# Kernel optimization log

Hardware: AMD Instinct MI355X
Metric: run time of the kernel (lower is better)

## Reference

```python
import jax, jax.numpy as jnp
import numpy as np

DIMS = 1024
HEAD = 16
HD = DIMS // HEAD          # head_dim = 64
LAYER = 2
STRIDE = max(1, 6 - LAYER)  # skip-path k/v stride = 4
EPS = 1.1920929e-07         # torch.finfo(float32).eps (RMSNorm eps=None default)


def rmsnorm(x, w):
    # torch nn.RMSNorm over last dim with affine weight
    ms = jnp.mean(jnp.square(x), axis=-1, keepdims=True)
    return x * jax.lax.rsqrt(ms + EPS) * w


def rope_freqs(seq_len):
    # rotary._compute_freqs with mask=None, x=None (mel-style scale)
    end = 2595.0 * np.log10(1.0 + 4000.0 / 200.0)
    scale = jnp.power(10.0, jnp.linspace(0.0, end, HD // 2, dtype=jnp.float32) / 2595.0) - 1.0
    base = 200.0 * scale / 1000.0                      # [HD//2]
    t = jnp.arange(seq_len, dtype=jnp.float32)          # [c]
    return t[:, None] * base[None, :]                   # [c, HD//2]


def rope(x, freqs):
    # x: [b,h,c,d]; interleaved pairs rotated by angle freqs[c, d//2]
    xr = x.reshape(*x.shape[:-1], HD // 2, 2)
    a, b = xr[..., 0], xr[..., 1]
    cos, sin = jnp.cos(freqs), jnp.sin(freqs)           # broadcast over [b,h]
    out = jnp.stack([a * cos - b * sin, a * sin + b * cos], axis=-1)
    return out.reshape(x.shape)


def setup_inputs() -> dict:
    key = jax.random.key(0)
    ks = jax.random.split(key, 4)
    d = DIMS
    init = lambda k, shape: jax.random.normal(k, shape, jnp.float32) * 0.02
    return {
        "x": jax.random.normal(ks[0], (4, 2048, d), jnp.float32),
        "rmsq_w": jnp.ones((d,), jnp.float32),
        "q_w": init(ks[1], (d, d)),
        "q_b": jnp.zeros((d,), jnp.float32),
        "rmskv_w": jnp.ones((d,), jnp.float32),
        "kv_w": init(ks[2], (d, 2 * d)),
        "kv_b": jnp.zeros((2 * d,), jnp.float32),
        "ln_w": jnp.ones((HD,), jnp.float32),
        "out_w": init(ks[3], (d, d)),
        "out_b": jnp.zeros((d,), jnp.float32),
    }


def reference(x, rmsq_w, q_w, q_b, rmskv_w, kv_w, kv_b, ln_w, out_w, out_b):
    b, c, d = x.shape
    # q = RMSNorm -> Linear -> [b,h,c,hd]
    q = (rmsnorm(x, rmsq_w) @ q_w + q_b).reshape(b, c, HEAD, HD).transpose(0, 2, 1, 3)
    # kv = RMSNorm -> Linear(d,2d) -> split last dim as (kv=2, h, hd)
    kv = (rmsnorm(x, rmskv_w) @ kv_w + kv_b).reshape(b, c, 2, HEAD, HD)
    k = kv[:, :, 0].transpose(0, 2, 1, 3)  # [b,h,c,hd]
    v = kv[:, :, 1].transpose(0, 2, 1, 3)
    # rotary embedding (full hd rotated since freqs cover hd//2 pairs)
    freqs = rope_freqs(c)
    q = rope(q, freqs)
    k = rope(k, freqs)
    # skip branch: strided subsampling of k/v (stride = max(1, 6-layer) = 4)
    k = k[:, :, ::STRIDE, :]
    v = v[:, :, ::STRIDE, :]
    # per-head RMSNorm on q/k, then SDPA (is_causal=False since mask=None)
    qn = rmsnorm(q, ln_w)
    kn = rmsnorm(k, ln_w)
    scores = jnp.einsum('bhqd,bhkd->bhqk', qn, kn) / jnp.sqrt(jnp.float32(HD))
    a = jnp.einsum('bhqk,bhkd->bhqd', jax.nn.softmax(scores, axis=-1), v)
    # out projection: [b,h,c,hd] -> [b,c,d] -> Linear
    out = a.transpose(0, 2, 1, 3).reshape(b, c, d) @ out_w + out_b
    return out
```

## Files before the change

### kernel.cpp

```cpp
#include <hip/hip_runtime.h>

#define EPSF 1.1920929e-07f
#define QSCALE 0.18033688011112042f

typedef _Float16 hf;
typedef __attribute__((ext_vector_type(4))) _Float16 h4;
typedef __attribute__((ext_vector_type(8))) _Float16 h8;
typedef __attribute__((ext_vector_type(4))) float fx4;

#define DEVI __device__ __forceinline__

DEVI void async16(const void* g, void* l) {
  __builtin_amdgcn_global_load_lds((const __attribute__((address_space(1))) unsigned int*)g,
                                   (__attribute__((address_space(3))) unsigned int*)l, 16, 0, 0);
}

DEVI fx4 mfma16(h4 a, h4 b, fx4 c) {
  return __builtin_amdgcn_mfma_f32_16x16x16f16(a, b, c, 0, 0, 0);
}
DEVI fx4 mfma32(h8 a, h8 b, fx4 c) {
  return __builtin_amdgcn_mfma_f32_16x16x32_f16(a, b, c, 0, 0, 0);
}

DEVI h8 ld16(const hf* base, int row, int g16) {
  int off = (row * 128 + (g16 << 4)) ^ ((row & 7) << 4);
  return *(const h8*)((const char*)base + off);
}
DEVI h4 ld8(const hf* base, int row, int g8) {
  int off = (row * 128 + (g8 << 3)) ^ ((row & 7) << 4);
  return *(const h4*)((const char*)base + off);
}

__global__ __launch_bounds__(256) void k_wcast(const float* __restrict__ W, hf* __restrict__ Wt,
                                               int K, int N) {
  __shared__ float ls[64][65];
  int kt = blockIdx.x, nt = blockIdx.y, t = threadIdx.x;
  int c4 = (t & 15) * 4, r0 = t >> 4;
#pragma unroll
  for (int i = 0; i < 4; ++i) {
    int row = i * 16 + r0;
    fx4 v = *(const fx4*)(W + (size_t)(kt * 64 + row) * N + nt * 64 + c4);
    ls[row][c4 + 0] = v[0]; ls[row][c4 + 1] = v[1];
    ls[row][c4 + 2] = v[2]; ls[row][c4 + 3] = v[3];
  }
  __syncthreads();
  int cc = t >> 4, kk4 = (t & 15) * 4;
#pragma unroll
  for (int i = 0; i < 4; ++i) {
    int nn = i * 16 + cc;
    h4 p = {(hf)ls[kk4 + 0][nn], (hf)ls[kk4 + 1][nn], (hf)ls[kk4 + 2][nn], (hf)ls[kk4 + 3][nn]};
    *(h4*)(Wt + (size_t)(nt * 64 + nn) * K + kt * 64 + kk4) = p;
  }
}

__global__ __launch_bounds__(256) void k_table(float* __restrict__ tab) {
  int idx = blockIdx.x * 256 + threadIdx.x;
  int tt = idx >> 5, j = idx & 31;
  double e = pow(21.0, (double)j / 31.0) - 1.0;
  float bf = (float)(0.2 * e);
  float fr = (float)tt * bf;
  double d = (double)fr;
  float2 cs = make_float2((float)cos(d), (float)sin(d));
  ((float2*)tab)[idx] = cs;
}

__global__ __launch_bounds__(256) void k_dualnorm(const float* __restrict__ x,
                                                  const float* __restrict__ wq,
                                                  const float* __restrict__ wkv,
                                                  hf* __restrict__ xqn, hf* __restrict__ xkvc) {
  int row = blockIdx.x, t = threadIdx.x;
  const fx4* xr = (const fx4*)(x + (size_t)row * 1024);
  fx4 v = xr[t];
  float ss = v[0] * v[0] + v[1] * v[1] + v[2] * v[2] + v[3] * v[3];
#pragma unroll
  for (int m = 1; m <= 32; m <<= 1) ss += __shfl_xor(ss, m);
  __shared__ float red[4];
  if ((t & 63) == 0) red[t >> 6] = ss;
  __syncthreads();
  float r = rsqrtf((red[0] + red[1] + red[2] + red[3]) * (1.0f / 1024.0f) + EPSF);
  fx4 a = ((const fx4*)wq)[t];
  h4 oq = {(hf)(v[0] * r * a[0]), (hf)(v[1] * r * a[1]), (hf)(v[2] * r * a[2]), (hf)(v[3] * r * a[3])};
  *(h4*)(xqn + (size_t)row * 1024 + t * 4) = oq;
  int c = row & 2047;
  if ((c & 3) == 0) {
    fx4 bk = ((const fx4*)wkv)[t];
    int crow = (row >> 11) * 512 + (c >> 2);
    h4 ok = {(hf)(v[0] * r * bk[0]), (hf)(v[1] * r * bk[1]), (hf)(v[2] * r * bk[2]), (hf)(v[3] * r * bk[3])};
    *(h4*)(xkvc + (size_t)crow * 1024 + t * 4) = ok;
  }
}

template <int EPI>
__global__ __launch_bounds__(256) void k_gemm(const hf* __restrict__ A, const hf* __restrict__ Bt,
                                              const float* __restrict__ bias, void* __restrict__ outp,
                                              int M, int N, int K, int MB, hf* __restrict__ vt) {
  __shared__ alignas(16) hf lsA[2][128 * 64];
  __shared__ alignas(16) hf lsB[2][128 * 64];
  int t = threadIdx.x, l = t & 63, w = t >> 6, grp = l >> 4, ln = l & 15;
  int bm = blockIdx.x % MB, bn = blockIdx.x / MB;
  int m0 = bm * 128, n0 = bn * 128;
  int wr = w >> 1, wc = w & 1;
  fx4 acc[4][4] = {};
  int nkt = K >> 6;

  auto stage = [&](int kt, int b) {
    int k0 = kt << 6;
#pragma unroll
    for (int p = 0; p < 4; ++p) {
      int ci = p * 256 + t;
      int row = ci >> 3, g = (ci & 7) ^ (row & 7);
      async16(A + (size_t)(m0 + row) * K + k0 + g * 8, (char*)lsA[b] + p * 4096 + w * 1024);
    }
#pragma unroll
    for (int p = 0; p < 4; ++p) {
      int ci = p * 256 + t;
      int row = ci >> 3, g = (ci & 7) ^ (row & 7);
      async16(Bt + (size_t)(n0 + row) * K + k0 + g * 8, (char*)lsB[b] + p * 4096 + w * 1024);
    }
  };

  stage(0, 0);
  __syncthreads();
  for (int kt = 0; kt < nkt; ++kt) {
    int cur = kt & 1;
    if (kt + 1 < nkt) stage(kt + 1, cur ^ 1);
    __builtin_amdgcn_sched_barrier(0);
#pragma unroll
    for (int kk = 0; kk < 2; ++kk) {
      h8 af[4], bf[4];
#pragma unroll
      for (int i = 0; i < 4; ++i) af[i] = ld16(lsA[cur], wr * 64 + i * 16 + ln, kk * 4 + grp);
#pragma unroll
      for (int i = 0; i < 4; ++i) bf[i] = ld16(lsB[cur], wc * 64 + i * 16 + ln, kk * 4 + grp);
#pragma unroll
      for (int mi = 0; mi < 4; ++mi)
#pragma unroll
        for (int ni = 0; ni < 4; ++ni)
          acc[mi][ni] = mfma32(af[mi], bf[ni], acc[mi][ni]);
    }
    __syncthreads();
  }
#pragma unroll
  for (int ni = 0; ni < 4; ++ni) {
    int n = n0 + wc * 64 + ni * 16 + ln;
    float bs = bias[n];
#pragma unroll
    for (int mi = 0; mi < 4; ++mi) {
      int mb_ = m0 + wr * 64 + mi * 16 + grp * 4;
      fx4 v = acc[mi][ni];
      v += bs;
      if constexpr (EPI == 2) {
        float* O = (float*)outp;
#pragma unroll
        for (int r = 0; r < 4; ++r) O[(size_t)(mb_ + r) * N + n] = v[r];
      } else if constexpr (EPI == 0) {
        hf* O = (hf*)outp;
#pragma unroll
        for (int r = 0; r < 4; ++r) O[(size_t)(mb_ + r) * N + n] = (hf)v[r];
      } else {
        if (n < 1024) {
          hf* O = (hf*)outp;
#pragma unroll
          for (int r = 0; r < 4; ++r) O[(size_t)(mb_ + r) * 1024 + n] = (hf)v[r];
        } else {
          int nv = n - 1024, h = nv >> 6, hd = nv & 63;
          int b = m0 >> 9, kc0 = mb_ & 511;
          h4 pk = {(hf)v[0], (hf)v[1], (hf)v[2], (hf)v[3]};
          *(h4*)(vt + ((size_t)(b * 16 + h) * 64 + hd) * 512 + kc0) = pk;
        }
      }
    }
  }
}

template <bool ISQ>
__global__ __launch_bounds__(256) void k_post(const hf* __restrict__ raw, const float* __restrict__ lnw,
                                              const float* __restrict__ tab, hf* __restrict__ outn) {
  int row = blockIdx.x, t = threadIdx.x;
  int h = t >> 4, hd0 = (t & 15) * 4;
  h4 q = ((const h4*)(raw + (size_t)row * 1024))[t];
  float q0 = (float)q[0], q1 = (float)q[1], q2 = (float)q[2], q3 = (float)q[3];
  float ss = q0 * q0 + q1 * q1 + q2 * q2 + q3 * q3;
  ss += __shfl_xor(ss, 1); ss += __shfl_xor(ss, 2);
  ss += __shfl_xor(ss, 4); ss += __shfl_xor(ss, 8);
  float scl = rsqrtf(ss * (1.0f / 64.0f) + EPSF);
  if (ISQ) scl *= QSCALE;
  int b, c, seq;
  if (ISQ) { b = row >> 11; c = row & 2047; seq = c; }
  else     { b = row >> 9;  c = row & 511;  seq = c * 4; }
  fx4 cs = *(const fx4*)(tab + (size_t)seq * 64 + hd0);
  float o0 = q0 * cs[0] - q1 * cs[1];
  float o1 = q0 * cs[1] + q1 * cs[0];
  float o2 = q2 * cs[2] - q3 * cs[3];
  float o3 = q2 * cs[3] + q3 * cs[2];
  fx4 lw = *(const fx4*)(lnw + hd0);
  h4 o = {(hf)(o0 * lw[0] * scl), (hf)(o1 * lw[1] * scl), (hf)(o2 * lw[2] * scl), (hf)(o3 * lw[3] * scl)};
  int rows = ISQ ? 2048 : 512;
  *(h4*)(outn + ((size_t)(b * 16 + h) * rows + c) * 64 + hd0) = o;
}

__global__ __launch_bounds__(256) void k_attn(const hf* __restrict__ qn, const hf* __restrict__ kn,
                                              const hf* __restrict__ vt, hf* __restrict__ a) {
  __shared__ alignas(16) hf lsK[2][64 * 64];
  __shared__ alignas(16) hf lsV[2][64 * 64];
  int t = threadIdx.x, l = t & 63, w = t >> 6, grp = l >> 4, ln = l & 15;
  int bq = blockIdx.x & 15, plane = blockIdx.x >> 4;
  const hf* qp = qn + (size_t)plane * 2048 * 64;
  const hf* kp = kn + (size_t)plane * 512 * 64;
  const hf* vp = vt + (size_t)plane * 64 * 512;
  int q0 = bq * 128 + w * 32;

  h8 qf[2][2];
#pragma unroll
  for (int mf = 0; mf < 2; ++mf)
#pragma unroll
    for (int kk = 0; kk < 2; ++kk)
      qf[mf][kk] = *(const h8*)(qp + (size_t)(q0 + mf * 16 + ln) * 64 + kk * 32 + grp * 8);

  fx4 o[4][2] = {};
  float mrun[2] = {-1e30f, -1e30f}, lrun[2] = {0.f, 0.f};

  auto stageKV = [&](int ch, int b) {
    int kc0 = ch * 64;
#pragma unroll
    for (int p = 0; p < 2; ++p) {
      int ci = p * 256 + t;
      int row = ci >> 3, g = (ci & 7) ^ (row & 7);
      async16(kp + (size_t)(kc0 + row) * 64 + g * 8, (char*)lsK[b] + p * 4096 + w * 1024);
    }
#pragma unroll
    for (int p = 0; p < 2; ++p) {
      int ci = p * 256 + t;
      int row = ci >> 3, g = (ci & 7) ^ (row & 7);
      async16(vp + (size_t)row * 512 + kc0 + g * 8, (char*)lsV[b] + p * 4096 + w * 1024);
    }
  };

  stageKV(0, 0);
  __syncthreads();

  for (int ch = 0; ch < 8; ++ch) {
    int cur = ch & 1;
    if (ch < 7) stageKV(ch + 1, cur ^ 1);
    __builtin_amdgcn_sched_barrier(0);

    fx4 s[4][2] = {};
#pragma unroll
    for (int kk = 0; kk < 2; ++kk) {
      h8 kf[4];
#pragma unroll
      for (int kt = 0; kt < 4; ++kt) kf[kt] = ld16(lsK[cur], kt * 16 + ln, kk * 4 + grp);
#pragma unroll
      for (int kt = 0; kt < 4; ++kt)
#pragma unroll
        for (int mf = 0; mf < 2; ++mf)
          s[kt][mf] = mfma32(kf[kt], qf[mf][kk], s[kt][mf]);
    }

#pragma unroll
    for (int mf = 0; mf < 2; ++mf) {
      float cm = -1e30f;
#pragma unroll
      for (int kt = 0; kt < 4; ++kt) {
        fx4 sv = s[kt][mf];
        cm = fmaxf(fmaxf(cm, fmaxf(sv[0], sv[1])), fmaxf(sv[2], sv[3]));
      }
      cm = fmaxf(cm, __shfl_xor(cm, 16));
      cm = fmaxf(cm, __shfl_xor(cm, 32));
      if (__any(cm > mrun[mf] + 8.0f)) {
        float mn = fmaxf(mrun[mf], cm);
        float al = __builtin_amdgcn_exp2f(mrun[mf] - mn);
        mrun[mf] = mn;
        lrun[mf] *= al;
#pragma unroll
        for (int nh = 0; nh < 4; ++nh) o[nh][mf] *= al;
      }
    }

    float ps[2] = {0.f, 0.f};
    h4 pf[4][2];
#pragma unroll
    for (int kt = 0; kt < 4; ++kt)
#pragma unroll
      for (int mf = 0; mf < 2; ++mf) {
        fx4 sv = s[kt][mf];
        float e0 = __builtin_amdgcn_exp2f(sv[0] - mrun[mf]);
        float e1 = __builtin_amdgcn_exp2f(sv[1] - mrun[mf]);
        float e2 = __builtin_amdgcn_exp2f(sv[2] - mrun[mf]);
        float e3 = __builtin_amdgcn_exp2f(sv[3] - mrun[mf]);
        ps[mf] += (e0 + e1) + (e2 + e3);
        h4 tp = {(hf)e0, (hf)e1, (hf)e2, (hf)e3};
        pf[kt][mf] = tp;
      }
#pragma unroll
    for (int mf = 0; mf < 2; ++mf) {
      float p2 = ps[mf];
      p2 += __shfl_xor(p2, 16);
      p2 += __shfl_xor(p2, 32);
      lrun[mf] += p2;
    }

#pragma unroll
    for (int ks = 0; ks < 4; ++ks) {
      h4 vf[4];
#pragma unroll
      for (int nh = 0; nh < 4; ++nh) vf[nh] = ld8(lsV[cur], nh * 16 + ln, ks * 4 + grp);
#pragma unroll
      for (int nh = 0; nh < 4; ++nh)
#pragma unroll
        for (int mf = 0; mf < 2; ++mf)
          o[nh][mf] = mfma16(vf[nh], pf[ks][mf], o[nh][mf]);
    }
    __syncthreads();
  }

  int b = plane >> 4, h = plane & 15;
#pragma unroll
  for (int mf = 0; mf < 2; ++mf) {
    float inv = 1.0f / lrun[mf];
    int cpos = q0 + mf * 16 + ln;
    size_t rowo = ((size_t)b * 2048 + cpos) * 1024;
#pragma unroll
    for (int nh = 0; nh < 4; ++nh) {
      h4 pk = {(hf)(o[nh][mf][0] * inv), (hf)(o[nh][mf][1] * inv),
               (hf)(o[nh][mf][2] * inv), (hf)(o[nh][mf][3] * inv)};
      *(h4*)(a + rowo + h * 64 + nh * 16 + grp * 4) = pk;
    }
  }
}

extern "C" void kernel_launch(void* const* d_in, const int* in_sizes, int n_in,
                              void* d_out, int out_size, void* d_ws, size_t ws_size,
                              hipStream_t stream) {
  (void)in_sizes; (void)n_in; (void)out_size; (void)ws_size;
  const float* x      = (const float*)d_in[0];
  const float* rmsq_w = (const float*)d_in[1];
  const float* q_w    = (const float*)d_in[2];
  const float* q_b    = (const float*)d_in[3];
  const float* rmskv_w= (const float*)d_in[4];
  const float* kv_w   = (const float*)d_in[5];
  const float* kv_b   = (const float*)d_in[6];
  const float* ln_w   = (const float*)d_in[7];
  const float* out_w  = (const float*)d_in[8];
  const float* out_b  = (const float*)d_in[9];

  char* ws = (char*)d_ws;
  hf* wqT   = (hf*)(ws + (size_t)0);
  hf* wkvT  = (hf*)(ws + ((size_t)2 << 20));
  hf* woT   = (hf*)(ws + ((size_t)6 << 20));
  float* tab= (float*)(ws + ((size_t)8 << 20));
  hf* xqn   = (hf*)(ws + ((size_t)9 << 20));
  hf* qn    = xqn;
  hf* xkvc  = (hf*)(ws + ((size_t)25 << 20));
  hf* qraw  = (hf*)(ws + ((size_t)29 << 20));
  hf* abuf  = qraw;
  hf* kraw  = (hf*)(ws + ((size_t)45 << 20));
  hf* kn    = (hf*)(ws + ((size_t)49 << 20));
  hf* vt    = (hf*)(ws + ((size_t)53 << 20));

  k_wcast<<<dim3(16, 16), 256, 0, stream>>>(q_w,   wqT,  1024, 1024);
  k_wcast<<<dim3(16, 32), 256, 0, stream>>>(kv_w,  wkvT, 1024, 2048);
  k_wcast<<<dim3(16, 16), 256, 0, stream>>>(out_w, woT,  1024, 1024);
  k_table<<<256, 256, 0, stream>>>(tab);
  k_dualnorm<<<8192, 256, 0, stream>>>(x, rmsq_w, rmskv_w, xqn, xkvc);
  k_gemm<0><<<64 * 8, 256, 0, stream>>>(xqn, wqT, q_b, qraw, 8192, 1024, 1024, 64, nullptr);
  k_gemm<1><<<16 * 16, 256, 0, stream>>>(xkvc, wkvT, kv_b, kraw, 2048, 2048, 1024, 16, vt);
  k_post<true><<<8192, 256, 0, stream>>>(qraw, ln_w, tab, qn);
  k_post<false><<<2048, 256, 0, stream>>>(kraw, ln_w, tab, kn);
  k_attn<<<1024, 256, 0, stream>>>(qn, kn, vt, abuf);
  k_gemm<2><<<64 * 8, 256, 0, stream>>>(abuf, woT, out_b, d_out, 8192, 1024, 1024, 64, nullptr);
}
```

Baseline: 233.4 us.

## Use partial vmcnt waits, setprio around MFMA, and XCD-aware tile remap in attention

The GEMM and attention loops drop the full __syncthreads drains. Each now waits with s_waitcnt vmcnt(N) only for the current stage's async LDS loads, so prefetches of the next stage stay in flight across the barrier. MFMA sections are wrapped in s_setprio to favour compute waves. The attention kernel also remaps block indices so consecutive tiles of a plane land on the same XCD for L2 reuse, and moves the Q fragment load after the first KV prefetch so the two overlap. The hand-counted vmcnt values depend on the exact number of outstanding loads, which is fragile if the compiler reorders or adds memory ops.

Result: no change. 230.9 us (-1.1%).

```diff
diff --git a/kernel.cpp b/kernel.cpp
--- a/kernel.cpp
+++ b/kernel.cpp
@@ -120,11 +120,17 @@
   };
 
   stage(0, 0);
-  __syncthreads();
   for (int kt = 0; kt < nkt; ++kt) {
     int cur = kt & 1;
-    if (kt + 1 < nkt) stage(kt + 1, cur ^ 1);
+    if (kt + 1 < nkt) {
+      stage(kt + 1, cur ^ 1);
+      asm volatile("s_waitcnt vmcnt(8)" ::: "memory");
+    } else {
+      asm volatile("s_waitcnt vmcnt(0)" ::: "memory");
+    }
+    __builtin_amdgcn_s_barrier();
     __builtin_amdgcn_sched_barrier(0);
+    __builtin_amdgcn_s_setprio(1);
 #pragma unroll
     for (int kk = 0; kk < 2; ++kk) {
       h8 af[4], bf[4];
@@ -138,7 +144,9 @@
         for (int ni = 0; ni < 4; ++ni)
           acc[mi][ni] = mfma32(af[mi], bf[ni], acc[mi][ni]);
     }
-    __syncthreads();
+    __builtin_amdgcn_s_setprio(0);
+    __builtin_amdgcn_sched_barrier(0);
+    __builtin_amdgcn_s_barrier();
   }
 #pragma unroll
   for (int ni = 0; ni < 4; ++ni) {
@@ -204,22 +212,13 @@
   __shared__ alignas(16) hf lsK[2][64 * 64];
   __shared__ alignas(16) hf lsV[2][64 * 64];
   int t = threadIdx.x, l = t & 63, w = t >> 6, grp = l >> 4, ln = l & 15;
-  int bq = blockIdx.x & 15, plane = blockIdx.x >> 4;
+  int tile = (blockIdx.x & 7) * (gridDim.x >> 3) + (blockIdx.x >> 3);
+  int bq = tile & 15, plane = tile >> 4;
   const hf* qp = qn + (size_t)plane * 2048 * 64;
   const hf* kp = kn + (size_t)plane * 512 * 64;
   const hf* vp = vt + (size_t)plane * 64 * 512;
   int q0 = bq * 128 + w * 32;
 
-  h8 qf[2][2];
-#pragma unroll
-  for (int mf = 0; mf < 2; ++mf)
-#pragma unroll
-    for (int kk = 0; kk < 2; ++kk)
-      qf[mf][kk] = *(const h8*)(qp + (size_t)(q0 + mf * 16 + ln) * 64 + kk * 32 + grp * 8);
-
-  fx4 o[4][2] = {};
-  float mrun[2] = {-1e30f, -1e30f}, lrun[2] = {0.f, 0.f};
-
   auto stageKV = [&](int ch, int b) {
     int kc0 = ch * 64;
 #pragma unroll
@@ -237,14 +236,30 @@
   };
 
   stageKV(0, 0);
-  __syncthreads();
+
+  h8 qf[2][2];
+#pragma unroll
+  for (int mf = 0; mf < 2; ++mf)
+#pragma unroll
+    for (int kk = 0; kk < 2; ++kk)
+      qf[mf][kk] = *(const h8*)(qp + (size_t)(q0 + mf * 16 + ln) * 64 + kk * 32 + grp * 8);
+
+  fx4 o[4][2] = {};
+  float mrun[2] = {-1e30f, -1e30f}, lrun[2] = {0.f, 0.f};
 
   for (int ch = 0; ch < 8; ++ch) {
     int cur = ch & 1;
-    if (ch < 7) stageKV(ch + 1, cur ^ 1);
+    if (ch < 7) {
+      stageKV(ch + 1, cur ^ 1);
+      asm volatile("s_waitcnt vmcnt(4)" ::: "memory");
+    } else {
+      asm volatile("s_waitcnt vmcnt(0)" ::: "memory");
+    }
+    __builtin_amdgcn_s_barrier();
     __builtin_amdgcn_sched_barrier(0);
 
     fx4 s[4][2] = {};
+    __builtin_amdgcn_s_setprio(1);
 #pragma unroll
     for (int kk = 0; kk < 2; ++kk) {
       h8 kf[4];
@@ -256,6 +271,7 @@
         for (int mf = 0; mf < 2; ++mf)
           s[kt][mf] = mfma32(kf[kt], qf[mf][kk], s[kt][mf]);
     }
+    __builtin_amdgcn_s_setprio(0);
 
 #pragma unroll
     for (int mf = 0; mf < 2; ++mf) {
@@ -300,6 +316,7 @@
       lrun[mf] += p2;
     }
 
+    __builtin_amdgcn_s_setprio(1);
 #pragma unroll
     for (int ks = 0; ks < 4; ++ks) {
       h4 vf[4];
@@ -311,7 +328,9 @@
         for (int mf = 0; mf < 2; ++mf)
           o[nh][mf] = mfma16(vf[nh], pf[ks][mf], o[nh][mf]);
     }
-    __syncthreads();
+    __builtin_amdgcn_s_setprio(0);
+    __builtin_amdgcn_sched_barrier(0);
+    __builtin_amdgcn_s_barrier();
   }
 
   int b = plane >> 4, h = plane & 15;
```
